# Optimization experiments

Hardware: AMD Instinct MI355X
Metric: run time of the kernel (lower is better)

The kernel has to match this reference:

```python
import jax, jax.numpy as jnp
import numpy as np

B, LS, LT = 32, 64, 64
V_SRC, V_TGT = 32000, 32000
E, H = 512, 512


def setup_inputs() -> dict:
    key = jax.random.key(0)
    ks = jax.random.split(key, 16)
    s = 0.05
    inp = {
        "src": jax.random.randint(ks[0], (B, LS), 0, V_SRC),
        "tgt": jax.random.randint(ks[1], (B, LT), 0, V_TGT),
        # encoder params
        "enc_embed": jax.random.normal(ks[2], (V_SRC, E), jnp.float32) * s,
        "enc_wih": jax.random.normal(ks[3], (E, H), jnp.float32) * s,
        "enc_bih": jax.random.normal(ks[4], (H,), jnp.float32) * s,
        "enc_whh": jax.random.normal(ks[5], (H, H), jnp.float32) * s,
        "enc_bhh": jax.random.normal(ks[6], (H,), jnp.float32) * s,
        # decoder params
        "dec_embed": jax.random.normal(ks[7], (V_TGT, E), jnp.float32) * s,
        "dec_wih": jax.random.normal(ks[8], (E, H), jnp.float32) * s,
        "dec_bih": jax.random.normal(ks[9], (H,), jnp.float32) * s,
        "dec_whh": jax.random.normal(ks[10], (H, H), jnp.float32) * s,
        "dec_bhh": jax.random.normal(ks[11], (H,), jnp.float32) * s,
        "h2o_w": jax.random.normal(ks[12], (H, V_TGT), jnp.float32) * s,
        "h2o_b": jax.random.normal(ks[13], (V_TGT,), jnp.float32) * s,
    }
    return inp


def _rnn_scan(tokens, embed, wih, bih, whh, bhh, h0):
    # tokens: (N, L) int; returns (final hidden (N,H), all hiddens (L,N,H))
    xs = embed[tokens].transpose(1, 0, 2)  # (L, N, E)

    def step(h, x):
        h = jnp.tanh(x @ wih + bih + h @ whh + bhh)
        return h, h

    h_last, hs = jax.lax.scan(step, h0, xs)
    return h_last, hs


def reference(src, tgt, enc_embed, enc_wih, enc_bih, enc_whh, enc_bhh,
              dec_embed, dec_wih, dec_bih, dec_whh, dec_bhh, h2o_w, h2o_b):
    n = src.shape[0]
    h0 = jnp.zeros((n, enc_whh.shape[0]), dtype=enc_whh.dtype)
    # encoder: tanh RNN over src, keep only final hidden (teacher-forced training path)
    hidden, _ = _rnn_scan(src, enc_embed, enc_wih, enc_bih, enc_whh, enc_bhh, h0)
    # decoder: tanh RNN over tgt with teacher forcing
    _, dec_hs = _rnn_scan(tgt, dec_embed, dec_wih, dec_bih, dec_whh, dec_bhh, hidden)  # (Lt, N, H)
    # per-step h2o + LogSoftmax, batched over all steps at once (same math)
    logits = dec_hs @ h2o_w + h2o_b  # (Lt, N, V)
    outputs = jax.nn.log_softmax(logits, axis=-1).transpose(1, 0, 2)  # (N, Lt, V)
    return outputs
```

## Files before the change

### kernel.cpp

```cpp
#include <hip/hip_runtime.h>

#define Bd 32
#define Ld 64
#define Hd 512
#define Vd 32000

typedef __bf16 bf16_t;
typedef __bf16 bf16x8 __attribute__((ext_vector_type(8)));
typedef float  f32x4  __attribute__((ext_vector_type(4)));

__global__ void k_prep(
    const int* __restrict__ src, const int* __restrict__ tgt,
    const float* __restrict__ enc_embed, const float* __restrict__ enc_wih,
    const float* __restrict__ enc_bih, const float* __restrict__ enc_bhh,
    const float* __restrict__ dec_embed, const float* __restrict__ dec_wih,
    const float* __restrict__ dec_bih, const float* __restrict__ dec_bhh,
    float* __restrict__ Aenc, float* __restrict__ Adec,
    const float* __restrict__ w, bf16_t* __restrict__ wT,
    unsigned long long* __restrict__ encX, unsigned long long* __restrict__ decX)
{
    __shared__ __align__(16) char smraw[33024];
    const int tid = threadIdx.x;
    const int bid = blockIdx.x;

    if (bid < 256) {
        {
            unsigned wgi = ((unsigned)bid << 8) + tid;
            if (wgi < 32768) encX[wgi] = ~0ull;
            else             decX[wgi - 32768] = ~0ull;
        }
        float* sm  = (float*)smraw;
        int*  tokl = (int*)(smraw + 32768);
        const bool isDec = bid >= 128;
        const int rb = (isDec ? bid - 128 : bid) << 4;
        const int*   toks = isDec ? tgt : src;
        const float* emb  = isDec ? dec_embed : enc_embed;
        const float* wih  = isDec ? dec_wih : enc_wih;
        const float* bi   = isDec ? dec_bih : enc_bih;
        const float* bh   = isDec ? dec_bhh : enc_bhh;
        float*       A    = isDec ? Adec : Aenc;
        if (tid < 16) {
            int r = rb + tid;
            tokl[tid] = toks[(r & 31) * Ld + (r >> 5)];
        }
        __syncthreads();
        #pragma unroll
        for (int u = 0; u < 8; ++u) {
            int f = tid + (u << 8);
            int row = f >> 7, c4 = f & 127;
            ((float4*)sm)[f] = ((const float4*)(emb + (size_t)tokl[row] * Hd))[c4];
        }
        __syncthreads();
        const int j0 = tid, j1 = tid + 256;
        float acc0[16], acc1[16];
        #pragma unroll
        for (int r = 0; r < 16; ++r) { acc0[r] = 0.f; acc1[r] = 0.f; }
        #pragma unroll 4
        for (int k = 0; k < Hd; ++k) {
            float w0 = wih[(size_t)k * Hd + j0];
            float w1 = wih[(size_t)k * Hd + j1];
            #pragma unroll
            for (int r = 0; r < 16; ++r) {
                float x = sm[r * Hd + k];
                acc0[r] += x * w0;
                acc1[r] += x * w1;
            }
        }
        float bb0 = bi[j0] + bh[j0], bb1 = bi[j1] + bh[j1];
        #pragma unroll
        for (int r = 0; r < 16; ++r) {
            A[(size_t)(rb + r) * Hd + j0] = acc0[r] + bb0;
            A[(size_t)(rb + r) * Hd + j1] = acc1[r] + bb1;
        }
    } else {
        float (*ls)[65] = (float(*)[65])smraw;
        const int b2 = bid - 256;
        const int v0 = (b2 % 500) << 6;
        const int k0 = (b2 / 500) << 6;
        #pragma unroll
        for (int u = 0; u < 16; ++u) {
            int f = tid + (u << 8);
            int r = f >> 6, cc = f & 63;
            ls[r][cc] = w[(size_t)(k0 + r) * Vd + v0 + cc];
        }
        __syncthreads();
        #pragma unroll
        for (int u = 0; u < 16; ++u) {
            int f = tid + (u << 8);
            int vr = f >> 6, kk = f & 63;
            wT[(size_t)(v0 + vr) * Hd + k0 + kk] = (bf16_t)ls[kk][vr];
        }
    }
}

__global__ __launch_bounds__(256, 1) void k_rec(
    const float* __restrict__ enc_whh, const float* __restrict__ dec_whh,
    const float* __restrict__ Aenc, const float* __restrict__ Adec,
    unsigned long long* __restrict__ encX, unsigned long long* __restrict__ decX,
    bf16_t* __restrict__ dhsB)
{
    const int tid = threadIdx.x;
    const int bid = blockIdx.x;
    const int c = bid & 31, p = bid >> 5;
    const int q = tid >> 6, lane = tid & 63;
    const int l4 = lane & 15, g = lane >> 4;
    const int jb = p << 6;
    const int col = jb + (q << 4) + l4;
    const int i0 = g << 7;
    __shared__ float hl[2][Hd];

    {
        float wE[128];
        #pragma unroll
        for (int i = 0; i < 128; ++i) wE[i] = enc_whh[(size_t)(i0 + i) * Hd + col];
        for (int t = 0; t < Ld; ++t) {
            const int par = (t + 1) & 1;
            float aval = (lane < 16) ? Aenc[(size_t)(t * Bd + c) * Hd + col] : 0.f;
            if (t == 0) {
                hl[par][tid] = 0.f; hl[par][tid + 256] = 0.f;
            } else {
                const unsigned long long* xs = encX + (size_t)(((t - 1) & 1) * Bd + c) * Hd;
                const unsigned want = (unsigned)(t - 1);
                unsigned long long v0 = __hip_atomic_load(xs + tid,       __ATOMIC_RELAXED, __HIP_MEMORY_SCOPE_AGENT);
                unsigned long long v1 = __hip_atomic_load(xs + tid + 256, __ATOMIC_RELAXED, __HIP_MEMORY_SCOPE_AGENT);
                while ((unsigned)(v0 >> 32) != want || (unsigned)(v1 >> 32) != want) {
                    __builtin_amdgcn_s_sleep(1);
                    if ((unsigned)(v0 >> 32) != want)
                        v0 = __hip_atomic_load(xs + tid,       __ATOMIC_RELAXED, __HIP_MEMORY_SCOPE_AGENT);
                    if ((unsigned)(v1 >> 32) != want)
                        v1 = __hip_atomic_load(xs + tid + 256, __ATOMIC_RELAXED, __HIP_MEMORY_SCOPE_AGENT);
                }
                union { unsigned u; float f; } c0, c1;
                c0.u = (unsigned)v0; c1.u = (unsigned)v1;
                hl[par][tid] = c0.f; hl[par][tid + 256] = c1.f;
            }
            __syncthreads();
            const float4* h4 = (const float4*)(&hl[par][i0]);
            float acc = 0.f;
            #pragma unroll
            for (int i = 0; i < 32; ++i) {
                float4 hv = h4[i];
                acc += wE[4*i]*hv.x + wE[4*i+1]*hv.y + wE[4*i+2]*hv.z + wE[4*i+3]*hv.w;
            }
            acc += __shfl_xor(acc, 16, 64);
            acc += __shfl_xor(acc, 32, 64);
            if (lane < 16) {
                float h = tanhf(aval + acc);
                union { float f; unsigned u; } cv; cv.f = h;
                unsigned long long pv = ((unsigned long long)(unsigned)t << 32) | cv.u;
                __hip_atomic_store(encX + (size_t)((t & 1) * Bd + c) * Hd + col, pv,
                                   __ATOMIC_RELAXED, __HIP_MEMORY_SCOPE_AGENT);
            }
        }
    }
    {
        float wD[128];
        #pragma unroll
        for (int i = 0; i < 128; ++i) wD[i] = dec_whh[(size_t)(i0 + i) * Hd + col];
        for (int s = 0; s < Ld; ++s) {
            const int par = (s + 1) & 1;
            float aval = (lane < 16) ? Adec[(size_t)(s * Bd + c) * Hd + col] : 0.f;
            {
                const unsigned long long* xs = (s == 0)
                    ? (encX + (size_t)(((Ld - 1) & 1) * Bd + c) * Hd)
                    : (decX + (size_t)(((s - 1) & 1) * Bd + c) * Hd);
                const unsigned want = (s == 0) ? (unsigned)(Ld - 1) : (unsigned)(64 + s - 1);
                unsigned long long v0 = __hip_atomic_load(xs + tid,       __ATOMIC_RELAXED, __HIP_MEMORY_SCOPE_AGENT);
                unsigned long long v1 = __hip_atomic_load(xs + tid + 256, __ATOMIC_RELAXED, __HIP_MEMORY_SCOPE_AGENT);
                while ((unsigned)(v0 >> 32) != want || (unsigned)(v1 >> 32) != want) {
                    __builtin_amdgcn_s_sleep(1);
                    if ((unsigned)(v0 >> 32) != want)
                        v0 = __hip_atomic_load(xs + tid,       __ATOMIC_RELAXED, __HIP_MEMORY_SCOPE_AGENT);
                    if ((unsigned)(v1 >> 32) != want)
                        v1 = __hip_atomic_load(xs + tid + 256, __ATOMIC_RELAXED, __HIP_MEMORY_SCOPE_AGENT);
                }
                union { unsigned u; float f; } c0, c1;
                c0.u = (unsigned)v0; c1.u = (unsigned)v1;
                hl[par][tid] = c0.f; hl[par][tid + 256] = c1.f;
            }
            __syncthreads();
            const float4* h4 = (const float4*)(&hl[par][i0]);
            float acc = 0.f;
            #pragma unroll
            for (int i = 0; i < 32; ++i) {
                float4 hv = h4[i];
                acc += wD[4*i]*hv.x + wD[4*i+1]*hv.y + wD[4*i+2]*hv.z + wD[4*i+3]*hv.w;
            }
            acc += __shfl_xor(acc, 16, 64);
            acc += __shfl_xor(acc, 32, 64);
            if (lane < 16) {
                float h = tanhf(aval + acc);
                union { float f; unsigned u; } cv; cv.f = h;
                unsigned long long pv = ((unsigned long long)(unsigned)(64 + s) << 32) | cv.u;
                __hip_atomic_store(decX + (size_t)((s & 1) * Bd + c) * Hd + col, pv,
                                   __ATOMIC_RELAXED, __HIP_MEMORY_SCOPE_AGENT);
                dhsB[((size_t)c * Ld + s) * Hd + col] = (bf16_t)h;
            }
        }
    }
}

__global__ __launch_bounds__(256, 2) void k_gemm(
    const bf16_t* __restrict__ Amat, const bf16_t* __restrict__ Bmat,
    const float* __restrict__ bias, float* __restrict__ out,
    float2* __restrict__ part2)
{
    __shared__ bf16_t At[128 * 32];
    __shared__ bf16_t Bt[128 * 32];
    __shared__ float smM[128][2];
    __shared__ float smL[128][2];
    const int tid = threadIdx.x;
    const int n0 = blockIdx.x << 7;
    const int v0 = blockIdx.y << 7;
    const int w = tid >> 6, lane = tid & 63;
    const int l15 = lane & 15, q8 = lane >> 4;
    const int moff = (w & 1) << 6, voff = (w >> 1) << 6;

    f32x4 acc[4][4];
    #pragma unroll
    for (int mi = 0; mi < 4; ++mi)
        #pragma unroll
        for (int vi = 0; vi < 4; ++vi)
            acc[mi][vi] = f32x4{0.f, 0.f, 0.f, 0.f};

    for (int kb = 0; kb < 16; ++kb) {
        __syncthreads();
        #pragma unroll
        for (int u = 0; u < 2; ++u) {
            int f = tid + (u << 8);
            int row = f >> 2, sub = f & 3;
            int subw = sub ^ (row & 3);
            uint4 av = *(const uint4*)(Amat + ((size_t)(n0 + row) * Hd + (kb << 5) + (sub << 3)));
            *(uint4*)(At + row * 32 + (subw << 3)) = av;
            uint4 bv = *(const uint4*)(Bmat + ((size_t)(v0 + row) * Hd + (kb << 5) + (sub << 3)));
            *(uint4*)(Bt + row * 32 + (subw << 3)) = bv;
        }
        __syncthreads();
        bf16x8 af[4], bfr[4];
        #pragma unroll
        for (int mi = 0; mi < 4; ++mi) {
            int m = moff + (mi << 4) + l15;
            af[mi] = *(const bf16x8*)(At + m * 32 + (((q8 ^ (m & 3)) & 3) << 3));
        }
        #pragma unroll
        for (int vi = 0; vi < 4; ++vi) {
            int vv = voff + (vi << 4) + l15;
            bfr[vi] = *(const bf16x8*)(Bt + vv * 32 + (((q8 ^ (vv & 3)) & 3) << 3));
        }
        #pragma unroll
        for (int mi = 0; mi < 4; ++mi)
            #pragma unroll
            for (int vi = 0; vi < 4; ++vi)
                acc[mi][vi] = __builtin_amdgcn_mfma_f32_16x16x32_bf16(af[mi], bfr[vi], acc[mi][vi], 0, 0, 0);
    }

    float bz[4];
    #pragma unroll
    for (int vi = 0; vi < 4; ++vi) bz[vi] = bias[v0 + voff + (vi << 4) + l15];

    float rm[16], rl[16];
    #pragma unroll
    for (int k = 0; k < 16; ++k) rm[k] = -3.4e38f;
    #pragma unroll
    for (int mi = 0; mi < 4; ++mi)
        #pragma unroll
        for (int r = 0; r < 4; ++r)
            #pragma unroll
            for (int vi = 0; vi < 4; ++vi)
                rm[mi * 4 + r] = fmaxf(rm[mi * 4 + r], acc[mi][vi][r] + bz[vi]);
    #pragma unroll
    for (int mask = 1; mask < 16; mask <<= 1)
        #pragma unroll
        for (int k = 0; k < 16; ++k)
            rm[k] = fmaxf(rm[k], __shfl_xor(rm[k], mask, 64));
    #pragma unroll
    for (int k = 0; k < 16; ++k) rl[k] = 0.f;
    #pragma unroll
    for (int vi = 0; vi < 4; ++vi) {
        int col = v0 + voff + (vi << 4) + l15;
        #pragma unroll
        for (int mi = 0; mi < 4; ++mi) {
            int row = n0 + moff + (mi << 4) + (q8 << 2);
            #pragma unroll
            for (int r = 0; r < 4; ++r) {
                float z = acc[mi][vi][r] + bz[vi];
                out[(size_t)(row + r) * Vd + col] = z;
                rl[mi * 4 + r] += __expf(z - rm[mi * 4 + r]);
            }
        }
    }
    #pragma unroll
    for (int mask = 1; mask < 16; mask <<= 1)
        #pragma unroll
        for (int k = 0; k < 16; ++k)
            rl[k] += __shfl_xor(rl[k], mask, 64);

    if (l15 == 0) {
        int half = w >> 1;
        #pragma unroll
        for (int mi = 0; mi < 4; ++mi)
            #pragma unroll
            for (int r = 0; r < 4; ++r) {
                int rloc = moff + (mi << 4) + (q8 << 2) + r;
                smM[rloc][half] = rm[mi * 4 + r];
                smL[rloc][half] = rl[mi * 4 + r];
            }
    }
    __syncthreads();
    if (tid < 128) {
        float m0 = smM[tid][0], m1 = smM[tid][1];
        float l0 = smL[tid][0], l1 = smL[tid][1];
        float M = fmaxf(m0, m1);
        float L = l0 * __expf(m0 - M) + l1 * __expf(m1 - M);
        part2[(size_t)blockIdx.y * 2048 + n0 + tid] = make_float2(M, L);
    }
}

__global__ void k_lsub(float* __restrict__ out, const float2* __restrict__ part2)
{
    const int n = blockIdx.x, tid = threadIdx.x;
    __shared__ float smx[256], sl[256];
    float m = -3.4e38f, l = 0.f;
    if (tid < 250) {
        float2 pp = part2[(size_t)tid * 2048 + n];
        m = pp.x; l = pp.y;
    }
    smx[tid] = m; sl[tid] = l;
    __syncthreads();
    for (int s2 = 128; s2 > 0; s2 >>= 1) {
        if (tid < s2) {
            float m1 = smx[tid], l1 = sl[tid];
            float m2 = smx[tid + s2], l2 = sl[tid + s2];
            float nm = fmaxf(m1, m2);
            sl[tid] = l1 * __expf(m1 - nm) + l2 * __expf(m2 - nm);
            smx[tid] = nm;
        }
        __syncthreads();
    }
    const float z = smx[0] + __logf(sl[0]);
    float4* row = (float4*)(out + (size_t)n * Vd);
    #pragma unroll 4
    for (int i = 0; i < 31; ++i) {
        int idx = i * 256 + tid;
        float4 x = row[idx];
        x.x -= z; x.y -= z; x.z -= z; x.w -= z;
        row[idx] = x;
    }
    if (tid < 64) {
        int idx = 7936 + tid;
        float4 x = row[idx];
        x.x -= z; x.y -= z; x.z -= z; x.w -= z;
        row[idx] = x;
    }
}

extern "C" void kernel_launch(void* const* d_in, const int* in_sizes, int n_in,
                              void* d_out, int out_size, void* d_ws, size_t ws_size,
                              hipStream_t stream)
{
    const int*   src       = (const int*)d_in[0];
    const int*   tgt       = (const int*)d_in[1];
    const float* enc_embed = (const float*)d_in[2];
    const float* enc_wih   = (const float*)d_in[3];
    const float* enc_bih   = (const float*)d_in[4];
    const float* enc_whh   = (const float*)d_in[5];
    const float* enc_bhh   = (const float*)d_in[6];
    const float* dec_embed = (const float*)d_in[7];
    const float* dec_wih   = (const float*)d_in[8];
    const float* dec_bih   = (const float*)d_in[9];
    const float* dec_whh   = (const float*)d_in[10];
    const float* dec_bhh   = (const float*)d_in[11];
    const float* h2o_w     = (const float*)d_in[12];
    const float* h2o_b     = (const float*)d_in[13];
    float* out = (float*)d_out;

    char* ws = (char*)d_ws;
    float*  Aenc  = (float*)(ws);
    float*  Adec  = (float*)(ws + ((size_t)4 << 20));
    unsigned long long* encX = (unsigned long long*)(ws + ((size_t)8 << 20));
    unsigned long long* decX = (unsigned long long*)(ws + ((size_t)8 << 20) + (256 << 10));
    bf16_t* dhsB  = (bf16_t*)(ws + ((size_t)9 << 20));
    bf16_t* wT    = (bf16_t*)(ws + ((size_t)12 << 20));
    float2* part2 = (float2*)(ws);

    k_prep<<<4256, 256, 0, stream>>>(src, tgt,
        enc_embed, enc_wih, enc_bih, enc_bhh,
        dec_embed, dec_wih, dec_bih, dec_bhh, Aenc, Adec,
        h2o_w, wT, encX, decX);
    k_rec<<<256, 256, 0, stream>>>(enc_whh, dec_whh, Aenc, Adec,
        encX, decX, dhsB);
    k_gemm<<<dim3(16, 250), 256, 0, stream>>>(dhsB, wT, h2o_b, out, part2);
    k_lsub<<<2048, 256, 0, stream>>>(out, part2);
}
```

Before: 858.4 us.

## Overlap weight transpose with recurrence, pad LDS hidden, prefetch GEMM tiles, remap grid

The h2o weight transpose/bf16 conversion moves from the prep kernel into the recurrence kernel as extra blocks, so it can run on CUs left idle by the 256 persistent recurrence blocks. Shared hidden-state storage is padded per 128-element chunk to avoid LDS bank conflicts in the matvec. The GEMM now register-prefetches the next K tile while computing the current one, and uses a 1D grid with a swizzled block order for L2 locality. The partial max/sum layout is transposed for coalesced reads in the log-softmax kernel. Risk: the extra blocks could delay scheduling of the persistent spin-waiting recurrence blocks (blocks 0-255 dispatch first, so this is likely fine).

```diff
diff --git a/kernel.cpp b/kernel.cpp
--- a/kernel.cpp
+++ b/kernel.cpp
@@ -8,6 +8,9 @@
 typedef __bf16 bf16_t;
 typedef __bf16 bf16x8 __attribute__((ext_vector_type(8)));
 typedef float  f32x4  __attribute__((ext_vector_type(4)));
+
+#define HCHUNK 132
+#define HIDX(e) ((((e) >> 7) * HCHUNK) + ((e) & 127))
 
 __global__ void k_prep(
     const int* __restrict__ src, const int* __restrict__ tgt,
@@ -16,64 +19,74 @@
     const float* __restrict__ dec_embed, const float* __restrict__ dec_wih,
     const float* __restrict__ dec_bih, const float* __restrict__ dec_bhh,
     float* __restrict__ Aenc, float* __restrict__ Adec,
-    const float* __restrict__ w, bf16_t* __restrict__ wT,
     unsigned long long* __restrict__ encX, unsigned long long* __restrict__ decX)
 {
-    __shared__ __align__(16) char smraw[33024];
+    __shared__ float sm[16 * Hd];
+    __shared__ int tokl[16];
     const int tid = threadIdx.x;
     const int bid = blockIdx.x;
 
-    if (bid < 256) {
-        {
-            unsigned wgi = ((unsigned)bid << 8) + tid;
-            if (wgi < 32768) encX[wgi] = ~0ull;
-            else             decX[wgi - 32768] = ~0ull;
-        }
-        float* sm  = (float*)smraw;
-        int*  tokl = (int*)(smraw + 32768);
-        const bool isDec = bid >= 128;
-        const int rb = (isDec ? bid - 128 : bid) << 4;
-        const int*   toks = isDec ? tgt : src;
-        const float* emb  = isDec ? dec_embed : enc_embed;
-        const float* wih  = isDec ? dec_wih : enc_wih;
-        const float* bi   = isDec ? dec_bih : enc_bih;
-        const float* bh   = isDec ? dec_bhh : enc_bhh;
-        float*       A    = isDec ? Adec : Aenc;
-        if (tid < 16) {
-            int r = rb + tid;
-            tokl[tid] = toks[(r & 31) * Ld + (r >> 5)];
-        }
-        __syncthreads();
-        #pragma unroll
-        for (int u = 0; u < 8; ++u) {
-            int f = tid + (u << 8);
-            int row = f >> 7, c4 = f & 127;
-            ((float4*)sm)[f] = ((const float4*)(emb + (size_t)tokl[row] * Hd))[c4];
-        }
-        __syncthreads();
-        const int j0 = tid, j1 = tid + 256;
-        float acc0[16], acc1[16];
-        #pragma unroll
-        for (int r = 0; r < 16; ++r) { acc0[r] = 0.f; acc1[r] = 0.f; }
-        #pragma unroll 4
-        for (int k = 0; k < Hd; ++k) {
-            float w0 = wih[(size_t)k * Hd + j0];
-            float w1 = wih[(size_t)k * Hd + j1];
-            #pragma unroll
-            for (int r = 0; r < 16; ++r) {
-                float x = sm[r * Hd + k];
-                acc0[r] += x * w0;
-                acc1[r] += x * w1;
-            }
-        }
-        float bb0 = bi[j0] + bh[j0], bb1 = bi[j1] + bh[j1];
+    {
+        unsigned wgi = ((unsigned)bid << 8) + tid;
+        if (wgi < 32768) encX[wgi] = ~0ull;
+        else             decX[wgi - 32768] = ~0ull;
+    }
+    const bool isDec = bid >= 128;
+    const int rb = (isDec ? bid - 128 : bid) << 4;
+    const int*   toks = isDec ? tgt : src;
+    const float* emb  = isDec ? dec_embed : enc_embed;
+    const float* wih  = isDec ? dec_wih : enc_wih;
+    const float* bi   = isDec ? dec_bih : enc_bih;
+    const float* bh   = isDec ? dec_bhh : enc_bhh;
+    float*       A    = isDec ? Adec : Aenc;
+    if (tid < 16) {
+        int r = rb + tid;
+        tokl[tid] = toks[(r & 31) * Ld + (r >> 5)];
+    }
+    __syncthreads();
+    #pragma unroll
+    for (int u = 0; u < 8; ++u) {
+        int f = tid + (u << 8);
+        int row = f >> 7, c4 = f & 127;
+        ((float4*)sm)[f] = ((const float4*)(emb + (size_t)tokl[row] * Hd))[c4];
+    }
+    __syncthreads();
+    const int j0 = tid, j1 = tid + 256;
+    float acc0[16], acc1[16];
+    #pragma unroll
+    for (int r = 0; r < 16; ++r) { acc0[r] = 0.f; acc1[r] = 0.f; }
+    #pragma unroll 4
+    for (int k = 0; k < Hd; ++k) {
+        float w0 = wih[(size_t)k * Hd + j0];
+        float w1 = wih[(size_t)k * Hd + j1];
         #pragma unroll
         for (int r = 0; r < 16; ++r) {
-            A[(size_t)(rb + r) * Hd + j0] = acc0[r] + bb0;
-            A[(size_t)(rb + r) * Hd + j1] = acc1[r] + bb1;
-        }
-    } else {
-        float (*ls)[65] = (float(*)[65])smraw;
+            float x = sm[r * Hd + k];
+            acc0[r] += x * w0;
+            acc1[r] += x * w1;
+        }
+    }
+    float bb0 = bi[j0] + bh[j0], bb1 = bi[j1] + bh[j1];
+    #pragma unroll
+    for (int r = 0; r < 16; ++r) {
+        A[(size_t)(rb + r) * Hd + j0] = acc0[r] + bb0;
+        A[(size_t)(rb + r) * Hd + j1] = acc1[r] + bb1;
+    }
+}
+
+__global__ __launch_bounds__(256, 1) void k_rec(
+    const float* __restrict__ enc_whh, const float* __restrict__ dec_whh,
+    const float* __restrict__ Aenc, const float* __restrict__ Adec,
+    unsigned long long* __restrict__ encX, unsigned long long* __restrict__ decX,
+    bf16_t* __restrict__ dhsB,
+    const float* __restrict__ w, bf16_t* __restrict__ wT)
+{
+    __shared__ float hl[2][4 * HCHUNK];
+    __shared__ float ls[64][65];
+    const int tid = threadIdx.x;
+    const int bid = blockIdx.x;
+
+    if (bid >= 256) {
         const int b2 = bid - 256;
         const int v0 = (b2 % 500) << 6;
         const int k0 = (b2 / 500) << 6;
@@ -90,34 +103,25 @@
             int vr = f >> 6, kk = f & 63;
             wT[(size_t)(v0 + vr) * Hd + k0 + kk] = (bf16_t)ls[kk][vr];
         }
-    }
-}
-
-__global__ __launch_bounds__(256, 1) void k_rec(
-    const float* __restrict__ enc_whh, const float* __restrict__ dec_whh,
-    const float* __restrict__ Aenc, const float* __restrict__ Adec,
-    unsigned long long* __restrict__ encX, unsigned long long* __restrict__ decX,
-    bf16_t* __restrict__ dhsB)
-{
-    const int tid = threadIdx.x;
-    const int bid = blockIdx.x;
+        return;
+    }
+
     const int c = bid & 31, p = bid >> 5;
     const int q = tid >> 6, lane = tid & 63;
     const int l4 = lane & 15, g = lane >> 4;
     const int jb = p << 6;
     const int col = jb + (q << 4) + l4;
-    const int i0 = g << 7;
-    __shared__ float hl[2][Hd];
+    const int hw0 = HIDX(tid), hw1 = HIDX(tid + 256);
 
     {
         float wE[128];
         #pragma unroll
-        for (int i = 0; i < 128; ++i) wE[i] = enc_whh[(size_t)(i0 + i) * Hd + col];
+        for (int i = 0; i < 128; ++i) wE[i] = enc_whh[(size_t)((g << 7) + i) * Hd + col];
         for (int t = 0; t < Ld; ++t) {
             const int par = (t + 1) & 1;
             float aval = (lane < 16) ? Aenc[(size_t)(t * Bd + c) * Hd + col] : 0.f;
             if (t == 0) {
-                hl[par][tid] = 0.f; hl[par][tid + 256] = 0.f;
+                hl[par][hw0] = 0.f; hl[par][hw1] = 0.f;
             } else {
                 const unsigned long long* xs = encX + (size_t)(((t - 1) & 1) * Bd + c) * Hd;
                 const unsigned want = (unsigned)(t - 1);
@@ -132,10 +136,10 @@
                 }
                 union { unsigned u; float f; } c0, c1;
                 c0.u = (unsigned)v0; c1.u = (unsigned)v1;
-                hl[par][tid] = c0.f; hl[par][tid + 256] = c1.f;
+                hl[par][hw0] = c0.f; hl[par][hw1] = c1.f;
             }
             __syncthreads();
-            const float4* h4 = (const float4*)(&hl[par][i0]);
+            const float4* h4 = (const float4*)(hl[par] + g * HCHUNK);
             float acc = 0.f;
             #pragma unroll
             for (int i = 0; i < 32; ++i) {
@@ -156,7 +160,7 @@
     {
         float wD[128];
         #pragma unroll
-        for (int i = 0; i < 128; ++i) wD[i] = dec_whh[(size_t)(i0 + i) * Hd + col];
+        for (int i = 0; i < 128; ++i) wD[i] = dec_whh[(size_t)((g << 7) + i) * Hd + col];
         for (int s = 0; s < Ld; ++s) {
             const int par = (s + 1) & 1;
             float aval = (lane < 16) ? Adec[(size_t)(s * Bd + c) * Hd + col] : 0.f;
@@ -176,10 +180,10 @@
                 }
                 union { unsigned u; float f; } c0, c1;
                 c0.u = (unsigned)v0; c1.u = (unsigned)v1;
-                hl[par][tid] = c0.f; hl[par][tid + 256] = c1.f;
+                hl[par][hw0] = c0.f; hl[par][hw1] = c1.f;
             }
             __syncthreads();
-            const float4* h4 = (const float4*)(&hl[par][i0]);
+            const float4* h4 = (const float4*)(hl[par] + g * HCHUNK);
             float acc = 0.f;
             #pragma unroll
             for (int i = 0; i < 32; ++i) {
@@ -210,8 +214,11 @@
     __shared__ float smM[128][2];
     __shared__ float smL[128][2];
     const int tid = threadIdx.x;
-    const int n0 = blockIdx.x << 7;
-    const int v0 = blockIdx.y << 7;
+    const int bid = blockIdx.x;
+    const int lin = (bid & 7) * 500 + (bid >> 3);
+    const int n0 = (lin & 15) << 7;
+    const int yv = lin >> 4;
+    const int v0 = yv << 7;
     const int w = tid >> 6, lane = tid & 63;
     const int l15 = lane & 15, q8 = lane >> 4;
     const int moff = (w & 1) << 6, voff = (w >> 1) << 6;
@@ -223,19 +230,29 @@
         for (int vi = 0; vi < 4; ++vi)
             acc[mi][vi] = f32x4{0.f, 0.f, 0.f, 0.f};
 
+    const int f0 = tid, f1 = tid + 256;
+    const int row0 = f0 >> 2, sub0 = f0 & 3, sw0 = sub0 ^ (row0 & 3);
+    const int row1 = f1 >> 2, sub1 = f1 & 3, sw1 = sub1 ^ (row1 & 3);
+    const bf16_t* aP0 = Amat + (size_t)(n0 + row0) * Hd + (sub0 << 3);
+    const bf16_t* aP1 = Amat + (size_t)(n0 + row1) * Hd + (sub1 << 3);
+    const bf16_t* bP0 = Bmat + (size_t)(v0 + row0) * Hd + (sub0 << 3);
+    const bf16_t* bP1 = Bmat + (size_t)(v0 + row1) * Hd + (sub1 << 3);
+
+    uint4 pa0 = *(const uint4*)(aP0), pa1 = *(const uint4*)(aP1);
+    uint4 pb0 = *(const uint4*)(bP0), pb1 = *(const uint4*)(bP1);
+
     for (int kb = 0; kb < 16; ++kb) {
         __syncthreads();
-        #pragma unroll
-        for (int u = 0; u < 2; ++u) {
-            int f = tid + (u << 8);
-            int row = f >> 2, sub = f & 3;
-            int subw = sub ^ (row & 3);
-            uint4 av = *(const uint4*)(Amat + ((size_t)(n0 + row) * Hd + (kb << 5) + (sub << 3)));
-            *(uint4*)(At + row * 32 + (subw << 3)) = av;
-            uint4 bv = *(const uint4*)(Bmat + ((size_t)(v0 + row) * Hd + (kb << 5) + (sub << 3)));
-            *(uint4*)(Bt + row * 32 + (subw << 3)) = bv;
-        }
+        *(uint4*)(At + row0 * 32 + (sw0 << 3)) = pa0;
+        *(uint4*)(At + row1 * 32 + (sw1 << 3)) = pa1;
+        *(uint4*)(Bt + row0 * 32 + (sw0 << 3)) = pb0;
+        *(uint4*)(Bt + row1 * 32 + (sw1 << 3)) = pb1;
         __syncthreads();
+        if (kb < 15) {
+            int ko = (kb + 1) << 5;
+            pa0 = *(const uint4*)(aP0 + ko); pa1 = *(const uint4*)(aP1 + ko);
+            pb0 = *(const uint4*)(bP0 + ko); pb1 = *(const uint4*)(bP1 + ko);
+        }
         bf16x8 af[4], bfr[4];
         #pragma unroll
         for (int mi = 0; mi < 4; ++mi) {
@@ -312,7 +329,7 @@
         float l0 = smL[tid][0], l1 = smL[tid][1];
         float M = fmaxf(m0, m1);
         float L = l0 * __expf(m0 - M) + l1 * __expf(m1 - M);
-        part2[(size_t)blockIdx.y * 2048 + n0 + tid] = make_float2(M, L);
+        part2[(size_t)(n0 + tid) * 250 + yv] = make_float2(M, L);
     }
 }
 
@@ -322,7 +339,7 @@
     __shared__ float smx[256], sl[256];
     float m = -3.4e38f, l = 0.f;
     if (tid < 250) {
-        float2 pp = part2[(size_t)tid * 2048 + n];
+        float2 pp = part2[(size_t)n * 250 + tid];
         m = pp.x; l = pp.y;
     }
     smx[tid] = m; sl[tid] = l;
@@ -383,12 +400,11 @@
     bf16_t* wT    = (bf16_t*)(ws + ((size_t)12 << 20));
     float2* part2 = (float2*)(ws);
 
-    k_prep<<<4256, 256, 0, stream>>>(src, tgt,
+    k_prep<<<256, 256, 0, stream>>>(src, tgt,
         enc_embed, enc_wih, enc_bih, enc_bhh,
-        dec_embed, dec_wih, dec_bih, dec_bhh, Aenc, Adec,
-        h2o_w, wT, encX, decX);
-    k_rec<<<256, 256, 0, stream>>>(enc_whh, dec_whh, Aenc, Adec,
-        encX, decX, dhsB);
-    k_gemm<<<dim3(16, 250), 256, 0, stream>>>(dhsB, wT, h2o_b, out, part2);
+        dec_embed, dec_wih, dec_bih, dec_bhh, Aenc, Adec, encX, decX);
+    k_rec<<<4256, 256, 0, stream>>>(enc_whh, dec_whh, Aenc, Adec,
+        encX, decX, dhsB, h2o_w, wT);
+    k_gemm<<<4000, 256, 0, stream>>>(dhsB, wT, h2o_b, out, part2);
     k_lsub<<<2048, 256, 0, stream>>>(out, part2);
 }
```

Measured after the change: 869.4 us. Within noise of the previous version (+1.3%).
